# Kernel tuning notes

Measured on AMD Instinct MI355X. Metric: run time of the kernel, lower is better.

The kernel has to match this reference:

```python
import jax, jax.numpy as jnp
import numpy as np

N_NODES = 50000
N_EDGES = 800000
D_FEAT = 128
HIDDEN = 128
OUT = 128


def setup_inputs() -> dict:
    key = jax.random.key(0)
    ks = jax.random.split(key, 8)
    sc_in = 1.0 / np.sqrt(D_FEAT)
    sc_h = 1.0 / np.sqrt(HIDDEN)
    return {
        "x": jax.random.normal(ks[0], (N_NODES, D_FEAT), dtype=jnp.float32),
        "edge_index": jax.random.randint(ks[1], (2, N_EDGES), 0, N_NODES, dtype=jnp.int64),
        "W1_l": jax.random.normal(ks[2], (D_FEAT, HIDDEN), dtype=jnp.float32) * sc_in,
        "b1_l": jnp.zeros((HIDDEN,), dtype=jnp.float32),
        "W1_r": jax.random.normal(ks[3], (D_FEAT, HIDDEN), dtype=jnp.float32) * sc_in,
        "W2_l": jax.random.normal(ks[4], (HIDDEN, OUT), dtype=jnp.float32) * sc_h,
        "b2_l": jnp.zeros((OUT,), dtype=jnp.float32),
        "W2_r": jax.random.normal(ks[5], (HIDDEN, OUT), dtype=jnp.float32) * sc_h,
    }


def _sage_conv(x, src, dst, W_l, b_l, W_r, n_nodes):
    # mean aggregation of source features onto destination nodes
    msgs = x[src]  # [E, d] irregular gather
    summed = jax.ops.segment_sum(msgs, dst, num_segments=n_nodes)
    cnt = jax.ops.segment_sum(jnp.ones((src.shape[0],), x.dtype), dst, num_segments=n_nodes)
    aggr = summed / jnp.maximum(cnt, 1.0)[:, None]  # empty neighborhoods -> 0
    # PyG SAGEConv: lin_l(aggr) + lin_r(x_root); bias lives on lin_l
    return aggr @ W_l + b_l + x @ W_r


def reference(x, edge_index, W1_l, b1_l, W1_r, W2_l, b2_l, W2_r):
    src, dst = edge_index[0], edge_index[1]
    n = x.shape[0]
    h = _sage_conv(x, src, dst, W1_l, b1_l, W1_r, n)
    h = jax.nn.relu(h)
    out = _sage_conv(h, src, dst, W2_l, b2_l, W2_r, n)
    return out
```

## Files before the change

kernel.cpp:

```cpp
#include <hip/hip_runtime.h>

#define NN 50000
#define NE 800000
#define D 128
#define SEGBITS 8
#define SEGSZ 256
#define NSEG 196
#define GRID_A 512
#define EPB ((NE + GRID_A - 1) / GRID_A)
#define FLAT (NSEG * GRID_A)
#define SBLK ((FLAT + 255) / 256)

typedef __attribute__((ext_vector_type(8))) short short8;
typedef __attribute__((ext_vector_type(4))) float f32x4;

__device__ inline unsigned short f2bf(float f) {
    unsigned u = __builtin_bit_cast(unsigned, f);
    unsigned r = (u + 0x7fffu + ((u >> 16) & 1u)) >> 16;
    return (unsigned short)r;
}
__device__ inline float bflo(unsigned u) { return __builtin_bit_cast(float, u << 16); }
__device__ inline float bfhi(unsigned u) { return __builtin_bit_cast(float, u & 0xffff0000u); }


__global__ __launch_bounds__(256) void histA_kernel(const int* __restrict__ dst,
        int* __restrict__ bh) {
    __shared__ int h[NSEG];
    int t = threadIdx.x;
    if (t < NSEG) h[t] = 0;
    __syncthreads();
    int beg = blockIdx.x * EPB;
    int end = min(beg + EPB, NE);
    for (int e = beg + t; e < end; e += 256) atomicAdd(&h[dst[e] >> SEGBITS], 1);
    __syncthreads();
    if (t < NSEG) bh[t * GRID_A + blockIdx.x] = h[t];
}

__global__ __launch_bounds__(256) void partialS_kernel(const int* __restrict__ bh,
        int* __restrict__ bsum) {
    __shared__ int s[256];
    int t = threadIdx.x;
    int i = blockIdx.x * 256 + t;
    s[t] = (i < FLAT) ? bh[i] : 0;
    __syncthreads();
    #pragma unroll
    for (int off = 128; off > 0; off >>= 1) {
        if (t < off) s[t] += s[t + off];
        __syncthreads();
    }
    if (t == 0) bsum[blockIdx.x] = s[0];
}

__global__ __launch_bounds__(512) void scanS_kernel(const int* __restrict__ bsum,
        int* __restrict__ boff) {
    __shared__ int s[512];
    int t = threadIdx.x;
    int v = (t < SBLK) ? bsum[t] : 0;
    s[t] = v;
    __syncthreads();
    #pragma unroll
    for (int off = 1; off < 512; off <<= 1) {
        int u = (t >= off) ? s[t - off] : 0;
        __syncthreads();
        s[t] += u;
        __syncthreads();
    }
    if (t < SBLK) boff[t] = s[t] - v;
}

__global__ __launch_bounds__(256) void scan2S_kernel(const int* __restrict__ bh,
        const int* __restrict__ boff, int* __restrict__ bases,
        int* __restrict__ segBase) {
    __shared__ int s[256];
    int t = threadIdx.x;
    int i = blockIdx.x * 256 + t;
    int v = (i < FLAT) ? bh[i] : 0;
    s[t] = v;
    __syncthreads();
    #pragma unroll
    for (int off = 1; off < 256; off <<= 1) {
        int u = (t >= off) ? s[t - off] : 0;
        __syncthreads();
        s[t] += u;
        __syncthreads();
    }
    if (i < FLAT) {
        int excl = s[t] - v + boff[blockIdx.x];
        bases[i] = excl;
        if ((i & (GRID_A - 1)) == 0) segBase[i >> 9] = excl;
    }
    if (i == 0) segBase[NSEG] = NE;
}

__global__ __launch_bounds__(256) void scatA_kernel(const int* __restrict__ src,
        const int* __restrict__ dst, const int* __restrict__ bases,
        unsigned* __restrict__ bucket) {
    __shared__ int cur[NSEG];
    int t = threadIdx.x;
    if (t < NSEG) cur[t] = bases[t * GRID_A + blockIdx.x];
    __syncthreads();
    int beg = blockIdx.x * EPB;
    int end = min(beg + EPB, NE);
    for (int e = beg + t; e < end; e += 256) {
        int d = dst[e];
        int sg = d >> SEGBITS;
        int p = atomicAdd(&cur[sg], 1);
        bucket[p] = ((unsigned)(d & (SEGSZ - 1)) << 24) | (unsigned)src[e];
    }
}

__global__ __launch_bounds__(256) void buildB_kernel(const unsigned* __restrict__ bucket,
        const int* __restrict__ segBase, int* __restrict__ rowptr, int* __restrict__ csr) {
    __shared__ int h[SEGSZ];
    __shared__ int s[SEGSZ];
    int sg = blockIdx.x;
    int t = threadIdx.x;
    int beg = segBase[sg], end = segBase[sg + 1];
    h[t] = 0;
    __syncthreads();
    for (int i = beg + t; i < end; i += 256) atomicAdd(&h[bucket[i] >> 24], 1);
    __syncthreads();
    int v = h[t];
    s[t] = v;
    __syncthreads();
    #pragma unroll
    for (int off = 1; off < 256; off <<= 1) {
        int u = (t >= off) ? s[t - off] : 0;
        __syncthreads();
        s[t] += u;
        __syncthreads();
    }
    int excl = beg + s[t] - v;
    int n = sg * SEGSZ + t;
    if (n <= NN) rowptr[n] = excl;
    h[t] = excl;
    __syncthreads();
    for (int i = beg + t; i < end; i += 256) {
        unsigned u = bucket[i];
        int p = atomicAdd(&h[u >> 24], 1);
        csr[p] = (int)(u & 0xFFFFFFu);
    }
}


__global__ __launch_bounds__(256) void prep_w_kernel(const float* __restrict__ W0,
        const float* __restrict__ W1, const float* __restrict__ W2,
        const float* __restrict__ W3, unsigned short* __restrict__ O) {
    int t = blockIdx.x * 256 + threadIdx.x;
    int w = t >> 11;
    int rem = t & 2047;
    int f = rem >> 6, l = rem & 63;
    int ct = f >> 2, kk = f & 3;
    int col = ct * 16 + (l & 15);
    int k0 = kk * 32 + (l >> 4) * 8;
    const float* W = (w == 0) ? W0 : (w == 1) ? W1 : (w == 2) ? W2 : W3;
    unsigned short* o = O + (size_t)w * 16384 + ((size_t)f * 64 + l) * 8;
    #pragma unroll
    for (int e = 0; e < 8; ++e) o[e] = f2bf(W[(k0 + e) * D + col]);
}


template<int AFP32>
__global__ __launch_bounds__(256, 1) void gemm_kernel(const void* __restrict__ Av,
        const unsigned short* __restrict__ WfL, const unsigned short* __restrict__ WfR,
        unsigned short* __restrict__ Yb, unsigned short* __restrict__ Zb, int nrows) {
    __shared__ short8 sW[4096];

    for (int i = threadIdx.x; i < 2048; i += 256) {
        sW[i]        = ((const short8*)WfL)[i];
        sW[i + 2048] = ((const short8*)WfR)[i];
    }
    __syncthreads();

    int wv = threadIdx.x >> 6, l = threadIdx.x & 63;
    int r15 = l & 15, kg = l >> 4;
    int row0 = blockIdx.x * 128 + wv * 32;

    short8 a[2][4];
    #pragma unroll
    for (int rt = 0; rt < 2; ++rt) {
        #pragma unroll
        for (int kk = 0; kk < 4; ++kk) {
            int row = row0 + rt * 16 + r15;
            row = min(row, nrows - 1);
            int off = kk * 32 + kg * 8;
            if (AFP32) {
                const float* A = (const float*)Av;
                float4 p = *(const float4*)(A + (size_t)row * D + off);
                float4 q = *(const float4*)(A + (size_t)row * D + off + 4);
                short8 v;
                v[0] = (short)f2bf(p.x); v[1] = (short)f2bf(p.y);
                v[2] = (short)f2bf(p.z); v[3] = (short)f2bf(p.w);
                v[4] = (short)f2bf(q.x); v[5] = (short)f2bf(q.y);
                v[6] = (short)f2bf(q.z); v[7] = (short)f2bf(q.w);
                a[rt][kk] = v;
            } else {
                const unsigned short* A = (const unsigned short*)Av;
                a[rt][kk] = *(const short8*)(A + (size_t)row * D + off);
            }
        }
    }

    f32x4 accY[2][8] = {};
    f32x4 accZ[2][8] = {};
    #pragma unroll
    for (int ct = 0; ct < 8; ++ct) {
        #pragma unroll
        for (int kk = 0; kk < 4; ++kk) {
            short8 bL = sW[(ct * 4 + kk) * 64 + l];
            short8 bR = sW[2048 + (ct * 4 + kk) * 64 + l];
            accY[0][ct] = __builtin_amdgcn_mfma_f32_16x16x32_bf16(a[0][kk], bL, accY[0][ct], 0, 0, 0);
            accY[1][ct] = __builtin_amdgcn_mfma_f32_16x16x32_bf16(a[1][kk], bL, accY[1][ct], 0, 0, 0);
            accZ[0][ct] = __builtin_amdgcn_mfma_f32_16x16x32_bf16(a[0][kk], bR, accZ[0][ct], 0, 0, 0);
            accZ[1][ct] = __builtin_amdgcn_mfma_f32_16x16x32_bf16(a[1][kk], bR, accZ[1][ct], 0, 0, 0);
        }
    }

    #pragma unroll
    for (int rt = 0; rt < 2; ++rt) {
        #pragma unroll
        for (int ct = 0; ct < 8; ++ct) {
            #pragma unroll
            for (int i = 0; i < 4; ++i) {
                int row = row0 + rt * 16 + kg * 4 + i;
                if (row < nrows) {
                    int col = ct * 16 + r15;
                    Yb[(size_t)row * D + col] = f2bf(accY[rt][ct][i]);
                    Zb[(size_t)row * D + col] = f2bf(accZ[rt][ct][i]);
                }
            }
        }
    }
}


template<int RELU, int OUTBF16>
__global__ __launch_bounds__(256) void agg_ep_kernel(const unsigned short* __restrict__ Yb,
        const unsigned short* __restrict__ Zb, const float* __restrict__ bias,
        const int* __restrict__ rowptr, const int* __restrict__ csr,
        void* __restrict__ outp) {
    int lane = threadIdx.x & 63;
    int wv = (blockIdx.x << 2) + (threadIdx.x >> 6);
    int nw = gridDim.x << 2;
    float b0 = bias[lane * 2], b1 = bias[lane * 2 + 1];

    for (int node = wv; node < NN; node += nw) {
        int beg = rowptr[node], end = rowptr[node + 1];
        float a0 = 0.f, a1 = 0.f;
        int j = beg;
        for (; j + 3 < end; j += 4) {
            int s0 = csr[j], s1 = csr[j + 1], s2 = csr[j + 2], s3 = csr[j + 3];
            unsigned u0 = *(const unsigned*)(Yb + (size_t)s0 * D + lane * 2);
            unsigned u1 = *(const unsigned*)(Yb + (size_t)s1 * D + lane * 2);
            unsigned u2 = *(const unsigned*)(Yb + (size_t)s2 * D + lane * 2);
            unsigned u3 = *(const unsigned*)(Yb + (size_t)s3 * D + lane * 2);
            a0 += bflo(u0) + bflo(u1) + bflo(u2) + bflo(u3);
            a1 += bfhi(u0) + bfhi(u1) + bfhi(u2) + bfhi(u3);
        }
        for (; j < end; ++j) {
            unsigned u = *(const unsigned*)(Yb + (size_t)csr[j] * D + lane * 2);
            a0 += bflo(u);
            a1 += bfhi(u);
        }
        float inv = (end > beg) ? 1.f / (float)(end - beg) : 0.f;
        unsigned uz = *(const unsigned*)(Zb + (size_t)node * D + lane * 2);
        float v0 = a0 * inv + b0 + bflo(uz);
        float v1 = a1 * inv + b1 + bfhi(uz);
        if (RELU) { v0 = fmaxf(v0, 0.f); v1 = fmaxf(v1, 0.f); }
        if (OUTBF16) {
            unsigned o = (unsigned)f2bf(v0) | ((unsigned)f2bf(v1) << 16);
            *(unsigned*)((unsigned short*)outp + (size_t)node * D + lane * 2) = o;
        } else {
            float2 o; o.x = v0; o.y = v1;
            *(float2*)((float*)outp + (size_t)node * D + lane * 2) = o;
        }
    }
}


extern "C" void kernel_launch(void* const* d_in, const int* in_sizes, int n_in,
                              void* d_out, int out_size, void* d_ws, size_t ws_size,
                              hipStream_t stream) {
    const float* x   = (const float*)d_in[0];
    const int*   ei  = (const int*)d_in[1];
    const float* W1l = (const float*)d_in[2];
    const float* b1  = (const float*)d_in[3];
    const float* W1r = (const float*)d_in[4];
    const float* W2l = (const float*)d_in[5];
    const float* b2  = (const float*)d_in[6];
    const float* W2r = (const float*)d_in[7];
    float* out = (float*)d_out;

    const int N = NN, E = NE;
    const int* src = ei;
    const int* dst = ei + E;

    char* ws = (char*)d_ws;
    size_t off = 0;
    auto alloc = [&](size_t bytes) -> void* {
        void* p = ws + off;
        off += (bytes + 255) & ~(size_t)255;
        return p;
    };
    int* rowptr  = (int*)alloc((size_t)(N + 1) * 4);
    int* csr     = (int*)alloc((size_t)E * 4);
    int* bh      = (int*)alloc((size_t)FLAT * 4);
    int* bases   = (int*)alloc((size_t)FLAT * 4);
    int* bsumS   = (int*)alloc((size_t)SBLK * 4);
    int* boffS   = (int*)alloc((size_t)SBLK * 4);
    int* segBase = (int*)alloc((size_t)(NSEG + 1) * 4);
    unsigned* bucket = (unsigned*)alloc((size_t)E * 4);
    unsigned short* hb  = (unsigned short*)alloc((size_t)N * D * 2);
    unsigned short* Yb  = (unsigned short*)alloc((size_t)N * D * 2);
    unsigned short* Zb  = (unsigned short*)alloc((size_t)N * D * 2);
    unsigned short* wf  = (unsigned short*)alloc((size_t)4 * 16384 * 2);

    histA_kernel<<<GRID_A, 256, 0, stream>>>(dst, bh);
    partialS_kernel<<<SBLK, 256, 0, stream>>>(bh, bsumS);
    scanS_kernel<<<1, 512, 0, stream>>>(bsumS, boffS);
    scan2S_kernel<<<SBLK, 256, 0, stream>>>(bh, boffS, bases, segBase);
    scatA_kernel<<<GRID_A, 256, 0, stream>>>(src, dst, bases, bucket);
    buildB_kernel<<<NSEG, 256, 0, stream>>>(bucket, segBase, rowptr, csr);

    prep_w_kernel<<<32, 256, 0, stream>>>(W1l, W1r, W2l, W2r, wf);

    unsigned short* wf1l = wf;
    unsigned short* wf1r = wf + 16384;
    unsigned short* wf2l = wf + 2 * 16384;
    unsigned short* wf2r = wf + 3 * 16384;

    int gblocks = (N + 127) / 128;

    gemm_kernel<1><<<gblocks, 256, 0, stream>>>(x, wf1l, wf1r, Yb, Zb, N);
    agg_ep_kernel<1, 1><<<2048, 256, 0, stream>>>(Yb, Zb, b1, rowptr, csr, hb);

    gemm_kernel<0><<<gblocks, 256, 0, stream>>>(hb, wf2l, wf2r, Yb, Zb, N);
    agg_ep_kernel<0, 0><<<2048, 256, 0, stream>>>(Yb, Zb, b2, rowptr, csr, out);
}
```

Before: 144.7 us.

## Fuse CSR build into one cooperative kernel and vectorize neighbor aggregation

Merges the seven CSR-construction and weight-prep launches into a single cooperative kernel that uses grid-wide syncs between phases, and halves the block count so the scan layout becomes 196x256. If the cooperative launch fails, it falls back to launching the same kernel six times, once per phase. The aggregation kernel now splits each wave into four 16-lane groups that each take a different edge, load 16-byte rows, and reduce across groups with shuffles. This cuts launch and inter-kernel gaps and widens the gather loads, at the cost of grid-sync overhead and fewer blocks in the edge-partition phases.

After: 295.0 us. 2.04x slower.

```diff
diff --git a/kernel.cpp b/kernel.cpp
--- a/kernel.cpp
+++ b/kernel.cpp
@@ -1,4 +1,7 @@
 #include <hip/hip_runtime.h>
+#include <hip/hip_cooperative_groups.h>
+
+namespace cg = cooperative_groups;
 
 #define NN 50000
 #define NE 800000
@@ -6,10 +9,9 @@
 #define SEGBITS 8
 #define SEGSZ 256
 #define NSEG 196
-#define GRID_A 512
-#define EPB ((NE + GRID_A - 1) / GRID_A)
-#define FLAT (NSEG * GRID_A)
-#define SBLK ((FLAT + 255) / 256)
+#define GRID_C 256
+#define EPB ((NE + GRID_C - 1) / GRID_C)
+#define FLAT (NSEG * GRID_C)
 
 typedef __attribute__((ext_vector_type(8))) short short8;
 typedef __attribute__((ext_vector_type(4))) float f32x4;
@@ -23,140 +25,124 @@
 __device__ inline float bfhi(unsigned u) { return __builtin_bit_cast(float, u & 0xffff0000u); }
 
 
-__global__ __launch_bounds__(256) void histA_kernel(const int* __restrict__ dst,
-        int* __restrict__ bh) {
-    __shared__ int h[NSEG];
-    int t = threadIdx.x;
-    if (t < NSEG) h[t] = 0;
-    __syncthreads();
-    int beg = blockIdx.x * EPB;
-    int end = min(beg + EPB, NE);
-    for (int e = beg + t; e < end; e += 256) atomicAdd(&h[dst[e] >> SEGBITS], 1);
-    __syncthreads();
-    if (t < NSEG) bh[t * GRID_A + blockIdx.x] = h[t];
-}
-
-__global__ __launch_bounds__(256) void partialS_kernel(const int* __restrict__ bh,
-        int* __restrict__ bsum) {
+__global__ __launch_bounds__(256) void coop_csr_kernel(
+        const int* __restrict__ src, const int* __restrict__ dst,
+        int* __restrict__ bh, int* __restrict__ bsum, int* __restrict__ boff,
+        int* __restrict__ bases, unsigned* __restrict__ bucket,
+        int* __restrict__ rowptr, int* __restrict__ csr,
+        const float* __restrict__ W0, const float* __restrict__ W1,
+        const float* __restrict__ W2, const float* __restrict__ W3,
+        unsigned short* __restrict__ wf, int phase) {
+    cg::grid_group grid = cg::this_grid();
+    __shared__ int h[256];
     __shared__ int s[256];
-    int t = threadIdx.x;
-    int i = blockIdx.x * 256 + t;
-    s[t] = (i < FLAT) ? bh[i] : 0;
-    __syncthreads();
-    #pragma unroll
-    for (int off = 128; off > 0; off >>= 1) {
-        if (t < off) s[t] += s[t + off];
-        __syncthreads();
-    }
-    if (t == 0) bsum[blockIdx.x] = s[0];
-}
-
-__global__ __launch_bounds__(512) void scanS_kernel(const int* __restrict__ bsum,
-        int* __restrict__ boff) {
-    __shared__ int s[512];
-    int t = threadIdx.x;
-    int v = (t < SBLK) ? bsum[t] : 0;
-    s[t] = v;
-    __syncthreads();
-    #pragma unroll
-    for (int off = 1; off < 512; off <<= 1) {
-        int u = (t >= off) ? s[t - off] : 0;
-        __syncthreads();
-        s[t] += u;
-        __syncthreads();
-    }
-    if (t < SBLK) boff[t] = s[t] - v;
-}
-
-__global__ __launch_bounds__(256) void scan2S_kernel(const int* __restrict__ bh,
-        const int* __restrict__ boff, int* __restrict__ bases,
-        int* __restrict__ segBase) {
-    __shared__ int s[256];
-    int t = threadIdx.x;
-    int i = blockIdx.x * 256 + t;
-    int v = (i < FLAT) ? bh[i] : 0;
-    s[t] = v;
-    __syncthreads();
-    #pragma unroll
-    for (int off = 1; off < 256; off <<= 1) {
-        int u = (t >= off) ? s[t - off] : 0;
-        __syncthreads();
-        s[t] += u;
-        __syncthreads();
-    }
-    if (i < FLAT) {
-        int excl = s[t] - v + boff[blockIdx.x];
-        bases[i] = excl;
-        if ((i & (GRID_A - 1)) == 0) segBase[i >> 9] = excl;
-    }
-    if (i == 0) segBase[NSEG] = NE;
-}
-
-__global__ __launch_bounds__(256) void scatA_kernel(const int* __restrict__ src,
-        const int* __restrict__ dst, const int* __restrict__ bases,
-        unsigned* __restrict__ bucket) {
-    __shared__ int cur[NSEG];
-    int t = threadIdx.x;
-    if (t < NSEG) cur[t] = bases[t * GRID_A + blockIdx.x];
-    __syncthreads();
-    int beg = blockIdx.x * EPB;
-    int end = min(beg + EPB, NE);
-    for (int e = beg + t; e < end; e += 256) {
-        int d = dst[e];
-        int sg = d >> SEGBITS;
-        int p = atomicAdd(&cur[sg], 1);
-        bucket[p] = ((unsigned)(d & (SEGSZ - 1)) << 24) | (unsigned)src[e];
-    }
-}
-
-__global__ __launch_bounds__(256) void buildB_kernel(const unsigned* __restrict__ bucket,
-        const int* __restrict__ segBase, int* __restrict__ rowptr, int* __restrict__ csr) {
-    __shared__ int h[SEGSZ];
-    __shared__ int s[SEGSZ];
-    int sg = blockIdx.x;
-    int t = threadIdx.x;
-    int beg = segBase[sg], end = segBase[sg + 1];
-    h[t] = 0;
-    __syncthreads();
-    for (int i = beg + t; i < end; i += 256) atomicAdd(&h[bucket[i] >> 24], 1);
-    __syncthreads();
-    int v = h[t];
-    s[t] = v;
-    __syncthreads();
-    #pragma unroll
-    for (int off = 1; off < 256; off <<= 1) {
-        int u = (t >= off) ? s[t - off] : 0;
-        __syncthreads();
-        s[t] += u;
-        __syncthreads();
-    }
-    int excl = beg + s[t] - v;
-    int n = sg * SEGSZ + t;
-    if (n <= NN) rowptr[n] = excl;
-    h[t] = excl;
-    __syncthreads();
-    for (int i = beg + t; i < end; i += 256) {
-        unsigned u = bucket[i];
-        int p = atomicAdd(&h[u >> 24], 1);
-        csr[p] = (int)(u & 0xFFFFFFu);
-    }
-}
-
-
-__global__ __launch_bounds__(256) void prep_w_kernel(const float* __restrict__ W0,
-        const float* __restrict__ W1, const float* __restrict__ W2,
-        const float* __restrict__ W3, unsigned short* __restrict__ O) {
-    int t = blockIdx.x * 256 + threadIdx.x;
-    int w = t >> 11;
-    int rem = t & 2047;
-    int f = rem >> 6, l = rem & 63;
-    int ct = f >> 2, kk = f & 3;
-    int col = ct * 16 + (l & 15);
-    int k0 = kk * 32 + (l >> 4) * 8;
-    const float* W = (w == 0) ? W0 : (w == 1) ? W1 : (w == 2) ? W2 : W3;
-    unsigned short* o = O + (size_t)w * 16384 + ((size_t)f * 64 + l) * 8;
-    #pragma unroll
-    for (int e = 0; e < 8; ++e) o[e] = f2bf(W[(k0 + e) * D + col]);
+    const bool all = (phase < 0);
+    int b = blockIdx.x, t = threadIdx.x;
+    int ebeg = b * EPB, eend = min(ebeg + EPB, NE);
+
+    if (all || phase == 0) {
+        h[t] = 0;
+        __syncthreads();
+        for (int e = ebeg + t; e < eend; e += 256) atomicAdd(&h[dst[e] >> SEGBITS], 1);
+        __syncthreads();
+        if (t < NSEG) bh[t * GRID_C + b] = h[t];
+        if (b < 32) {
+            int tg = b * 256 + t;
+            int w = tg >> 11, rem = tg & 2047;
+            int f = rem >> 6, l = rem & 63;
+            int ct = f >> 2, kk = f & 3;
+            int col = ct * 16 + (l & 15);
+            int k0 = kk * 32 + (l >> 4) * 8;
+            const float* W = (w == 0) ? W0 : (w == 1) ? W1 : (w == 2) ? W2 : W3;
+            unsigned short* o = wf + (size_t)w * 16384 + ((size_t)f * 64 + l) * 8;
+            #pragma unroll
+            for (int e = 0; e < 8; ++e) o[e] = f2bf(W[(k0 + e) * D + col]);
+        }
+    }
+    if (all) grid.sync();
+
+    if ((all || phase == 1) && b < NSEG) {
+        s[t] = bh[b * 256 + t];
+        __syncthreads();
+        #pragma unroll
+        for (int off = 128; off > 0; off >>= 1) {
+            if (t < off) s[t] += s[t + off];
+            __syncthreads();
+        }
+        if (t == 0) bsum[b] = s[0];
+    }
+    if (all) grid.sync();
+
+    if ((all || phase == 2) && b == 0) {
+        int v = (t < NSEG) ? bsum[t] : 0;
+        s[t] = v;
+        __syncthreads();
+        #pragma unroll
+        for (int off = 1; off < 256; off <<= 1) {
+            int u = (t >= off) ? s[t - off] : 0;
+            __syncthreads();
+            s[t] += u;
+            __syncthreads();
+        }
+        if (t < NSEG) boff[t] = s[t] - v;
+        if (t == NSEG - 1) boff[NSEG] = s[t];
+    }
+    if (all) grid.sync();
+
+    if ((all || phase == 3) && b < NSEG) {
+        int v = bh[b * 256 + t];
+        s[t] = v;
+        __syncthreads();
+        #pragma unroll
+        for (int off = 1; off < 256; off <<= 1) {
+            int u = (t >= off) ? s[t - off] : 0;
+            __syncthreads();
+            s[t] += u;
+            __syncthreads();
+        }
+        bases[b * 256 + t] = boff[b] + s[t] - v;
+    }
+    if (all) grid.sync();
+
+    if (all || phase == 4) {
+        if (t < NSEG) h[t] = bases[t * 256 + b];
+        __syncthreads();
+        for (int e = ebeg + t; e < eend; e += 256) {
+            int d = dst[e];
+            int sg = d >> SEGBITS;
+            int p = atomicAdd(&h[sg], 1);
+            bucket[p] = ((unsigned)(d & (SEGSZ - 1)) << 24) | (unsigned)src[e];
+        }
+    }
+    if (all) grid.sync();
+
+    if ((all || phase == 5) && b < NSEG) {
+        int sb = boff[b], se = boff[b + 1];
+        h[t] = 0;
+        __syncthreads();
+        for (int i = sb + t; i < se; i += 256) atomicAdd(&h[bucket[i] >> 24], 1);
+        __syncthreads();
+        int v = h[t];
+        s[t] = v;
+        __syncthreads();
+        #pragma unroll
+        for (int off = 1; off < 256; off <<= 1) {
+            int u = (t >= off) ? s[t - off] : 0;
+            __syncthreads();
+            s[t] += u;
+            __syncthreads();
+        }
+        int excl = sb + s[t] - v;
+        int n = b * SEGSZ + t;
+        if (n <= NN) rowptr[n] = excl;
+        h[t] = excl;
+        __syncthreads();
+        for (int i = sb + t; i < se; i += 256) {
+            unsigned u = bucket[i];
+            int p = atomicAdd(&h[u >> 24], 1);
+            csr[p] = (int)(u & 0xFFFFFFu);
+        }
+    }
 }
 
 
@@ -240,39 +226,60 @@
         const int* __restrict__ rowptr, const int* __restrict__ csr,
         void* __restrict__ outp) {
     int lane = threadIdx.x & 63;
+    int sub = lane >> 4;
+    int m = lane & 15;
     int wv = (blockIdx.x << 2) + (threadIdx.x >> 6);
     int nw = gridDim.x << 2;
-    float b0 = bias[lane * 2], b1 = bias[lane * 2 + 1];
+    float bb[8];
+    #pragma unroll
+    for (int e = 0; e < 8; ++e) bb[e] = bias[m * 8 + e];
 
     for (int node = wv; node < NN; node += nw) {
         int beg = rowptr[node], end = rowptr[node + 1];
-        float a0 = 0.f, a1 = 0.f;
-        int j = beg;
-        for (; j + 3 < end; j += 4) {
-            int s0 = csr[j], s1 = csr[j + 1], s2 = csr[j + 2], s3 = csr[j + 3];
-            unsigned u0 = *(const unsigned*)(Yb + (size_t)s0 * D + lane * 2);
-            unsigned u1 = *(const unsigned*)(Yb + (size_t)s1 * D + lane * 2);
-            unsigned u2 = *(const unsigned*)(Yb + (size_t)s2 * D + lane * 2);
-            unsigned u3 = *(const unsigned*)(Yb + (size_t)s3 * D + lane * 2);
-            a0 += bflo(u0) + bflo(u1) + bflo(u2) + bflo(u3);
-            a1 += bfhi(u0) + bfhi(u1) + bfhi(u2) + bfhi(u3);
-        }
-        for (; j < end; ++j) {
-            unsigned u = *(const unsigned*)(Yb + (size_t)csr[j] * D + lane * 2);
-            a0 += bflo(u);
-            a1 += bfhi(u);
-        }
-        float inv = (end > beg) ? 1.f / (float)(end - beg) : 0.f;
-        unsigned uz = *(const unsigned*)(Zb + (size_t)node * D + lane * 2);
-        float v0 = a0 * inv + b0 + bflo(uz);
-        float v1 = a1 * inv + b1 + bfhi(uz);
-        if (RELU) { v0 = fmaxf(v0, 0.f); v1 = fmaxf(v1, 0.f); }
-        if (OUTBF16) {
-            unsigned o = (unsigned)f2bf(v0) | ((unsigned)f2bf(v1) << 16);
-            *(unsigned*)((unsigned short*)outp + (size_t)node * D + lane * 2) = o;
-        } else {
-            float2 o; o.x = v0; o.y = v1;
-            *(float2*)((float*)outp + (size_t)node * D + lane * 2) = o;
+        float acc[8] = {};
+        for (int j = beg + sub; j < end; j += 4) {
+            int sn = csr[j];
+            uint4 u = *(const uint4*)(Yb + (size_t)sn * D + m * 8);
+            acc[0] += bflo(u.x); acc[1] += bfhi(u.x);
+            acc[2] += bflo(u.y); acc[3] += bfhi(u.y);
+            acc[4] += bflo(u.z); acc[5] += bfhi(u.z);
+            acc[6] += bflo(u.w); acc[7] += bfhi(u.w);
+        }
+        #pragma unroll
+        for (int e = 0; e < 8; ++e) {
+            acc[e] += __shfl_xor(acc[e], 16, 64);
+            acc[e] += __shfl_xor(acc[e], 32, 64);
+        }
+        if (sub == 0) {
+            float inv = (end > beg) ? 1.f / (float)(end - beg) : 0.f;
+            uint4 uz = *(const uint4*)(Zb + (size_t)node * D + m * 8);
+            float v[8];
+            v[0] = acc[0] * inv + bb[0] + bflo(uz.x);
+            v[1] = acc[1] * inv + bb[1] + bfhi(uz.x);
+            v[2] = acc[2] * inv + bb[2] + bflo(uz.y);
+            v[3] = acc[3] * inv + bb[3] + bfhi(uz.y);
+            v[4] = acc[4] * inv + bb[4] + bflo(uz.z);
+            v[5] = acc[5] * inv + bb[5] + bfhi(uz.z);
+            v[6] = acc[6] * inv + bb[6] + bflo(uz.w);
+            v[7] = acc[7] * inv + bb[7] + bfhi(uz.w);
+            if (RELU) {
+                #pragma unroll
+                for (int e = 0; e < 8; ++e) v[e] = fmaxf(v[e], 0.f);
+            }
+            if (OUTBF16) {
+                uint4 o;
+                o.x = (unsigned)f2bf(v[0]) | ((unsigned)f2bf(v[1]) << 16);
+                o.y = (unsigned)f2bf(v[2]) | ((unsigned)f2bf(v[3]) << 16);
+                o.z = (unsigned)f2bf(v[4]) | ((unsigned)f2bf(v[5]) << 16);
+                o.w = (unsigned)f2bf(v[6]) | ((unsigned)f2bf(v[7]) << 16);
+                *(uint4*)((unsigned short*)outp + (size_t)node * D + m * 8) = o;
+            } else {
+                float* op = (float*)outp + (size_t)node * D + m * 8;
+                float4 o1 = {v[0], v[1], v[2], v[3]};
+                float4 o2 = {v[4], v[5], v[6], v[7]};
+                *(float4*)op = o1;
+                *(float4*)(op + 4) = o2;
+            }
         }
     }
 }
@@ -305,24 +312,28 @@
     int* rowptr  = (int*)alloc((size_t)(N + 1) * 4);
     int* csr     = (int*)alloc((size_t)E * 4);
     int* bh      = (int*)alloc((size_t)FLAT * 4);
+    int* bsum    = (int*)alloc(256 * 4);
+    int* boff    = (int*)alloc(256 * 4);
     int* bases   = (int*)alloc((size_t)FLAT * 4);
-    int* bsumS   = (int*)alloc((size_t)SBLK * 4);
-    int* boffS   = (int*)alloc((size_t)SBLK * 4);
-    int* segBase = (int*)alloc((size_t)(NSEG + 1) * 4);
     unsigned* bucket = (unsigned*)alloc((size_t)E * 4);
     unsigned short* hb  = (unsigned short*)alloc((size_t)N * D * 2);
     unsigned short* Yb  = (unsigned short*)alloc((size_t)N * D * 2);
     unsigned short* Zb  = (unsigned short*)alloc((size_t)N * D * 2);
     unsigned short* wf  = (unsigned short*)alloc((size_t)4 * 16384 * 2);
 
-    histA_kernel<<<GRID_A, 256, 0, stream>>>(dst, bh);
-    partialS_kernel<<<SBLK, 256, 0, stream>>>(bh, bsumS);
-    scanS_kernel<<<1, 512, 0, stream>>>(bsumS, boffS);
-    scan2S_kernel<<<SBLK, 256, 0, stream>>>(bh, boffS, bases, segBase);
-    scatA_kernel<<<GRID_A, 256, 0, stream>>>(src, dst, bases, bucket);
-    buildB_kernel<<<NSEG, 256, 0, stream>>>(bucket, segBase, rowptr, csr);
-
-    prep_w_kernel<<<32, 256, 0, stream>>>(W1l, W1r, W2l, W2r, wf);
+    int phase_all = -1;
+    void* cargs[] = { (void*)&src, (void*)&dst, (void*)&bh, (void*)&bsum, (void*)&boff,
+                      (void*)&bases, (void*)&bucket, (void*)&rowptr, (void*)&csr,
+                      (void*)&W1l, (void*)&W1r, (void*)&W2l, (void*)&W2r,
+                      (void*)&wf, (void*)&phase_all };
+    hipError_t ce = hipLaunchCooperativeKernel((void*)coop_csr_kernel,
+            dim3(GRID_C), dim3(256), cargs, 0, stream);
+    if (ce != hipSuccess) {
+        (void)hipGetLastError();
+        for (int p = 0; p < 6; ++p)
+            coop_csr_kernel<<<GRID_C, 256, 0, stream>>>(src, dst, bh, bsum, boff,
+                    bases, bucket, rowptr, csr, W1l, W1r, W2l, W2r, wf, p);
+    }
 
     unsigned short* wf1l = wf;
     unsigned short* wf1r = wf + 16384;
```
